# Kernel tuning notes

Hardware: AMD Instinct MI355X
Metric: run time of the kernel (lower is better)

The kernel has to match this reference:

```python
import jax, jax.numpy as jnp
import numpy as np

N = 50000      # nodes
E = 600000     # edges
HID = 128      # hidden_dim
H = 8          # attn_heads
D = HID // H   # attn_dim = 16
CLAMP = 5.0
LN_EPS = 1e-5


def _xavier(key, shape, fan_in, fan_out):
    std = float(np.sqrt(2.0 / (fan_in + fan_out)))
    return jax.random.normal(key, shape, dtype=jnp.float32) * std


def setup_inputs() -> dict:
    key = jax.random.key(0)
    ks = jax.random.split(key, 32)
    x = jax.random.normal(ks[0], (N, HID), dtype=jnp.float32)
    conn = jax.random.normal(ks[1], (E, HID), dtype=jnp.float32)
    log_deg = jax.random.uniform(ks[2], (N, 1), dtype=jnp.float32) * 4.0
    edge_index = jax.random.randint(ks[3], (2, E), 0, N)
    # attention projections (torch Linear weight [out,in]; stored here as [in,out])
    WQ = _xavier(ks[4], (HID, HID), HID, HID)
    WK = _xavier(ks[5], (HID, HID), HID, HID)
    WV = _xavier(ks[6], (HID, HID), HID, HID)
    WE = _xavier(ks[7], (HID, 2 * HID), HID, 2 * HID)
    Aw = _xavier(ks[8], (D, H, 1), D, 1)
    Bw = _xavier(ks[9], (D, H, D), D, D)
    Ho_w = _xavier(ks[10], (HID, HID), HID, HID)
    Ho_b = jnp.zeros((HID,), jnp.float32)
    Eo_w = _xavier(ks[11], (HID, HID), HID, HID)
    Eo_b = jnp.zeros((HID,), jnp.float32)
    deg_coef = _xavier(ks[12], (1, HID, 2), HID, 2)
    ln1h_g = jnp.ones((HID,), jnp.float32); ln1h_b = jnp.zeros((HID,), jnp.float32)
    ln1e_g = jnp.ones((HID,), jnp.float32); ln1e_b = jnp.zeros((HID,), jnp.float32)
    ln2h_g = jnp.ones((HID,), jnp.float32); ln2h_b = jnp.zeros((HID,), jnp.float32)
    W1 = _xavier(ks[13], (HID, 2 * HID), HID, 2 * HID)
    b1 = jnp.zeros((2 * HID,), jnp.float32)
    W2 = _xavier(ks[14], (2 * HID, HID), 2 * HID, HID)
    b2 = jnp.zeros((HID,), jnp.float32)
    return dict(x=x, conn=conn, log_deg=log_deg, edge_index=edge_index,
                WQ=WQ, WK=WK, WV=WV, WE=WE, Aw=Aw, Bw=Bw,
                Ho_w=Ho_w, Ho_b=Ho_b, Eo_w=Eo_w, Eo_b=Eo_b, deg_coef=deg_coef,
                ln1h_g=ln1h_g, ln1h_b=ln1h_b, ln1e_g=ln1e_g, ln1e_b=ln1e_b,
                ln2h_g=ln2h_g, ln2h_b=ln2h_b, W1=W1, b1=b1, W2=W2, b2=b2)


def _signed_sqrt(c):
    # sqrt(relu(c)) - sqrt(relu(-c)), written nan-safe for grads
    pos = jnp.sqrt(jnp.where(c > 0, c, 1.0))
    neg = jnp.sqrt(jnp.where(c < 0, -c, 1.0))
    return jnp.where(c > 0, pos, 0.0) - jnp.where(c < 0, neg, 0.0)


def _layernorm(v, g, b):
    m = jnp.mean(v, axis=-1, keepdims=True)
    var = jnp.mean(jnp.square(v - m), axis=-1, keepdims=True)
    return (v - m) * jax.lax.rsqrt(var + LN_EPS) * g + b


def _forward(x, conn, log_deg, edge_index, WQ, WK, WV, WE, Aw, Bw,
             Ho_w, Ho_b, Eo_w, Eo_b, deg_coef,
             ln1h_g, ln1h_b, ln1e_g, ln1e_b, ln2h_g, ln2h_b, W1, b1, W2, b2):
    dst, src = edge_index[0], edge_index[1]
    Qh = x @ WQ          # [N, HID]
    Kh = x @ WK
    Vh = x @ WV
    Eh = conn @ WE       # [E, 2*HID]
    Ew, Eb = Eh[:, :HID], Eh[:, HID:]

    msg1 = Qh[dst] + Kh[src]                 # gather  [E, HID]
    conn_e = jax.nn.relu(_signed_sqrt(msg1 * Ew) + Eb)   # act='relu'
    e_attn = conn_e                          # Eo (edge output of attention)

    conn_r = conn_e.reshape(E, H, D)
    score = jnp.einsum('ehd,dhc->ehc', conn_r, Aw)       # [E, H, 1]
    score = jnp.clip(score, -CLAMP, CLAMP)
    # scatter softmax over dst
    smax = jax.ops.segment_max(score, dst, num_segments=N)
    score = jnp.exp(score - smax[dst])
    ssum = jax.ops.segment_sum(score, dst, num_segments=N)
    score = score / (ssum[dst] + 1e-16)

    Vsrc = Vh[src].reshape(E, H, D)
    agg = jax.ops.segment_sum(Vsrc * score, dst, num_segments=N)   # [N, H, D]
    rowV = jax.ops.segment_sum(conn_r * score, dst, num_segments=N)
    rowV = jnp.einsum('nhd,dhc->nhc', rowV, Bw)                    # [N, H, D]
    h_attn = Qh + (agg + rowV).reshape(N, HID)

    # outer layer (eval mode: no dropout)
    h = jnp.stack([h_attn, h_attn * log_deg], axis=-1)   # [N, HID, 2]
    h = jnp.sum(h * deg_coef, axis=-1)
    h = h @ Ho_w + Ho_b
    e = e_attn @ Eo_w + Eo_b
    h = x + h
    e = conn + e
    h = _layernorm(h, ln1h_g, ln1h_b)
    e = _layernorm(e, ln1e_g, ln1e_b)
    h_in2 = h
    h = jax.nn.relu(h @ W1 + b1) @ W2 + b2
    h = _layernorm(h_in2 + h, ln2h_g, ln2h_b)
    return h, e


def reference(x, conn, log_deg, edge_index, WQ, WK, WV, WE, Aw, Bw,
              Ho_w, Ho_b, Eo_w, Eo_b, deg_coef,
              ln1h_g, ln1h_b, ln1e_g, ln1e_b, ln2h_g, ln2h_b, W1, b1, W2, b2):
    return _forward(x, conn, log_deg, edge_index, WQ, WK, WV, WE, Aw, Bw,
                    Ho_w, Ho_b, Eo_w, Eo_b, deg_coef,
                    ln1h_g, ln1h_b, ln1e_g, ln1e_b, ln2h_g, ln2h_b, W1, b1, W2, b2)
```

## Files before the change

### kernel.cpp

```cpp
#include <hip/hip_runtime.h>
#include <hip/hip_bf16.h>

#define NN 50000
#define NE 600000
#define HIDC 128
#define NH 8
#define DH 16

typedef unsigned short u16;
typedef __attribute__((ext_vector_type(8))) short bf16x8;
typedef __attribute__((ext_vector_type(4))) float f32x4;

static __device__ __forceinline__ float bf2f(u16 u) {
    unsigned int x = ((unsigned int)u) << 16;
    return __uint_as_float(x);
}
static __device__ __forceinline__ u16 f2bf(float f) {
    unsigned int x = __float_as_uint(f);
    unsigned int r = (x + 0x7fffu + ((x >> 16) & 1u)) >> 16;
    return (u16)r;
}
static __device__ __forceinline__ void split2(float v, u16& h, u16& l) {
    h = f2bf(v);
    l = f2bf(v - bf2f(h));
}

__global__ void k_init(int* deg, int* cursor) {
    int i = blockIdx.x * blockDim.x + threadIdx.x;
    if (i < NN) { deg[i] = 0; cursor[i] = 0; }
}

__global__ void k_count(const int* __restrict__ ei, int* __restrict__ deg) {
    int e = blockIdx.x * blockDim.x + threadIdx.x;
    if (e < NE) atomicAdd(&deg[ei[e]], 1);
}

__global__ void k_scan(const int* __restrict__ deg, int* __restrict__ rowstart) {
    __shared__ int warpsum[16];
    __shared__ int chunkcarry;
    int t = threadIdx.x;
    int lane = t & 63, w = t >> 6;
    if (t == 0) { chunkcarry = 0; rowstart[0] = 0; }
    __syncthreads();
    for (int base = 0; base < NN; base += 4096) {
        int idx = base + t * 4;
        int v0 = (idx + 0 < NN) ? deg[idx + 0] : 0;
        int v1 = (idx + 1 < NN) ? deg[idx + 1] : 0;
        int v2 = (idx + 2 < NN) ? deg[idx + 2] : 0;
        int v3 = (idx + 3 < NN) ? deg[idx + 3] : 0;
        int s0 = v0, s1 = s0 + v1, s2 = s1 + v2, s3 = s2 + v3;
        int tot = s3;
        int sc = tot;
#pragma unroll
        for (int off = 1; off < 64; off <<= 1) {
            int u = __shfl_up(sc, off);
            if (lane >= off) sc += u;
        }
        if (lane == 63) warpsum[w] = sc;
        __syncthreads();
        int wpre = 0;
        for (int i = 0; i < w; i++) wpre += warpsum[i];
        int carry = chunkcarry;
        __syncthreads();
        int pre = carry + wpre + (sc - tot);
        if (idx + 0 < NN) rowstart[idx + 1] = pre + s0;
        if (idx + 1 < NN) rowstart[idx + 2] = pre + s1;
        if (idx + 2 < NN) rowstart[idx + 3] = pre + s2;
        if (idx + 3 < NN) rowstart[idx + 4] = pre + s3;
        if (t == 1023) chunkcarry = carry + wpre + sc;
        __syncthreads();
    }
}

__global__ void k_fill(const int* __restrict__ ei, const int* __restrict__ rowstart,
                       int* __restrict__ cursor, int* __restrict__ csr) {
    int e = blockIdx.x * blockDim.x + threadIdx.x;
    if (e < NE) {
        int d = ei[e];
        int slot = atomicAdd(&cursor[d], 1);
        csr[rowstart[d] + slot] = e;
    }
}

template <int NC, int K, bool RELU>
__global__ __launch_bounds__(256) void k_gemm(const float* __restrict__ A,
                                              const float* __restrict__ W,
                                              const float* __restrict__ bias,
                                              float* __restrict__ C, int M) {
    constexpr int NCT_W = NC / 32;
    __shared__ __align__(16) u16 Ah[4 * 64 * 8], Al[4 * 64 * 8];
    __shared__ __align__(16) u16 Bh[(NC / 16) * 64 * 8], Bl[(NC / 16) * 64 * 8];

    const int t = threadIdx.x;
    const int lane = t & 63, wid = t >> 6;
    const int wr = wid >> 1, wc = wid & 1;
    const int c15 = lane & 15, lg = lane >> 4;
    const int row0 = blockIdx.x * 64;

    f32x4 acc[2][NCT_W];
#pragma unroll
    for (int m = 0; m < 2; m++)
#pragma unroll
        for (int n = 0; n < NCT_W; n++) acc[m][n] = (f32x4){0.f, 0.f, 0.f, 0.f};

    for (int k0 = 0; k0 < K; k0 += 32) {
#pragma unroll
        for (int i = 0; i < 2; i++) {
            int fl = t * 2 + i;
            int r = fl >> 3, k4 = fl & 7;
            float4 v = make_float4(0.f, 0.f, 0.f, 0.f);
            int row = row0 + r;
            if (row < M) v = *(const float4*)(A + (size_t)row * K + k0 + k4 * 4);
            int base = ((r >> 4) * 64 + (r & 15) + ((k4 >> 1) << 4)) * 8 + (k4 & 1) * 4;
            u16 hx, lx, hy, ly, hz, lz, hw, lw;
            split2(v.x, hx, lx); split2(v.y, hy, ly);
            split2(v.z, hz, lz); split2(v.w, hw, lw);
            ushort4 ph; ph.x = hx; ph.y = hy; ph.z = hz; ph.w = hw;
            ushort4 pl; pl.x = lx; pl.y = ly; pl.z = lz; pl.w = lw;
            *(ushort4*)&Ah[base] = ph;
            *(ushort4*)&Al[base] = pl;
        }
#pragma unroll
        for (int hb = 0; hb < NC / 128; hb++) {
            int kb = (t >> 5) * 4;
            int c0 = hb * 128 + (t & 31) * 4;
            const float* wp = W + (size_t)(k0 + kb) * NC + c0;
            float4 w0 = *(const float4*)(wp);
            float4 w1 = *(const float4*)(wp + NC);
            float4 w2 = *(const float4*)(wp + 2 * NC);
            float4 w3 = *(const float4*)(wp + 3 * NC);
#pragma unroll
            for (int j = 0; j < 4; j++) {
                float e0 = j == 0 ? w0.x : j == 1 ? w0.y : j == 2 ? w0.z : w0.w;
                float e1 = j == 0 ? w1.x : j == 1 ? w1.y : j == 2 ? w1.z : w1.w;
                float e2 = j == 0 ? w2.x : j == 1 ? w2.y : j == 2 ? w2.z : w2.w;
                float e3 = j == 0 ? w3.x : j == 1 ? w3.y : j == 2 ? w3.z : w3.w;
                int c = c0 + j;
                int base = ((c >> 4) * 64 + (c & 15) + ((kb >> 3) << 4)) * 8 + (kb & 4);
                u16 h0, l0, h1, l1, h2, l2, h3, l3;
                split2(e0, h0, l0); split2(e1, h1, l1);
                split2(e2, h2, l2); split2(e3, h3, l3);
                ushort4 ph; ph.x = h0; ph.y = h1; ph.z = h2; ph.w = h3;
                ushort4 pl; pl.x = l0; pl.y = l1; pl.z = l2; pl.w = l3;
                *(ushort4*)&Bh[base] = ph;
                *(ushort4*)&Bl[base] = pl;
            }
        }
        __syncthreads();
        bf16x8 ah[2], alo[2];
#pragma unroll
        for (int m = 0; m < 2; m++) {
            int rt = wr * 2 + m;
            ah[m] = *(const bf16x8*)&Ah[(rt * 64 + lane) * 8];
            alo[m] = *(const bf16x8*)&Al[(rt * 64 + lane) * 8];
        }
#pragma unroll
        for (int n = 0; n < NCT_W; n++) {
            int ct = wc * NCT_W + n;
            bf16x8 bh = *(const bf16x8*)&Bh[(ct * 64 + lane) * 8];
            bf16x8 bl = *(const bf16x8*)&Bl[(ct * 64 + lane) * 8];
#pragma unroll
            for (int m = 0; m < 2; m++) {
                acc[m][n] = __builtin_amdgcn_mfma_f32_16x16x32_bf16(ah[m], bh, acc[m][n], 0, 0, 0);
                acc[m][n] = __builtin_amdgcn_mfma_f32_16x16x32_bf16(ah[m], bl, acc[m][n], 0, 0, 0);
                acc[m][n] = __builtin_amdgcn_mfma_f32_16x16x32_bf16(alo[m], bh, acc[m][n], 0, 0, 0);
            }
        }
        __syncthreads();
    }
#pragma unroll
    for (int m = 0; m < 2; m++) {
        int rbase = row0 + wr * 32 + m * 16 + lg * 4;
#pragma unroll
        for (int n = 0; n < NCT_W; n++) {
            int col = wc * (NCT_W * 16) + n * 16 + c15;
            float bv = bias ? bias[col] : 0.f;
#pragma unroll
            for (int r = 0; r < 4; r++) {
                int row = rbase + r;
                if (row < M) {
                    float o = acc[m][n][r] + bv;
                    if (RELU) o = fmaxf(o, 0.f);
                    C[(size_t)row * NC + col] = o;
                }
            }
        }
    }
}

__global__ __launch_bounds__(256) void k_edge_pre(
    const float* __restrict__ conn, const float* __restrict__ WE,
    const float* __restrict__ Qh, const float* __restrict__ Kh,
    const int* __restrict__ ei, const float* __restrict__ Aw,
    u16* __restrict__ conn_e, float* __restrict__ scoreraw) {
    __shared__ __align__(16) u16 Ah[4 * 64 * 8], Al[4 * 64 * 8];
    __shared__ __align__(16) u16 Bh[16 * 64 * 8], Bl[16 * 64 * 8];
    const int t = threadIdx.x;
    const int lane = t & 63, wid = t >> 6;
    const int wr = wid >> 1, wc = wid & 1;
    const int c15 = lane & 15, lg = lane >> 4;
    const int row0 = blockIdx.x * 64;

    f32x4 acc[2][8];
#pragma unroll
    for (int m = 0; m < 2; m++)
#pragma unroll
        for (int n = 0; n < 8; n++) acc[m][n] = (f32x4){0.f, 0.f, 0.f, 0.f};

    for (int k0 = 0; k0 < 128; k0 += 32) {
#pragma unroll
        for (int i = 0; i < 2; i++) {
            int fl = t * 2 + i;
            int r = fl >> 3, k4 = fl & 7;
            float4 v = *(const float4*)(conn + (size_t)(row0 + r) * 128 + k0 + k4 * 4);
            int base = ((r >> 4) * 64 + (r & 15) + ((k4 >> 1) << 4)) * 8 + (k4 & 1) * 4;
            u16 hx, lx, hy, ly, hz, lz, hw, lw;
            split2(v.x, hx, lx); split2(v.y, hy, ly);
            split2(v.z, hz, lz); split2(v.w, hw, lw);
            ushort4 ph; ph.x = hx; ph.y = hy; ph.z = hz; ph.w = hw;
            ushort4 pl; pl.x = lx; pl.y = ly; pl.z = lz; pl.w = lw;
            *(ushort4*)&Ah[base] = ph;
            *(ushort4*)&Al[base] = pl;
        }
#pragma unroll
        for (int hb = 0; hb < 2; hb++) {
            int kb = (t >> 5) * 4;
            int c0 = hb * 128 + (t & 31) * 4;
            const float* wp = WE + (size_t)(k0 + kb) * 256 + c0;
            float4 w0 = *(const float4*)(wp);
            float4 w1 = *(const float4*)(wp + 256);
            float4 w2 = *(const float4*)(wp + 512);
            float4 w3 = *(const float4*)(wp + 768);
#pragma unroll
            for (int j = 0; j < 4; j++) {
                float e0 = j == 0 ? w0.x : j == 1 ? w0.y : j == 2 ? w0.z : w0.w;
                float e1 = j == 0 ? w1.x : j == 1 ? w1.y : j == 2 ? w1.z : w1.w;
                float e2 = j == 0 ? w2.x : j == 1 ? w2.y : j == 2 ? w2.z : w2.w;
                float e3 = j == 0 ? w3.x : j == 1 ? w3.y : j == 2 ? w3.z : w3.w;
                int c = c0 + j;
                int base = ((c >> 4) * 64 + (c & 15) + ((kb >> 3) << 4)) * 8 + (kb & 4);
                u16 h0, l0, h1, l1, h2, l2, h3, l3;
                split2(e0, h0, l0); split2(e1, h1, l1);
                split2(e2, h2, l2); split2(e3, h3, l3);
                ushort4 ph; ph.x = h0; ph.y = h1; ph.z = h2; ph.w = h3;
                ushort4 pl; pl.x = l0; pl.y = l1; pl.z = l2; pl.w = l3;
                *(ushort4*)&Bh[base] = ph;
                *(ushort4*)&Bl[base] = pl;
            }
        }
        __syncthreads();
        bf16x8 ah[2], alo[2];
#pragma unroll
        for (int m = 0; m < 2; m++) {
            int rt = wr * 2 + m;
            ah[m] = *(const bf16x8*)&Ah[(rt * 64 + lane) * 8];
            alo[m] = *(const bf16x8*)&Al[(rt * 64 + lane) * 8];
        }
#pragma unroll
        for (int nn = 0; nn < 8; nn++) {
            int ct = (nn < 4) ? (wc * 4 + nn) : (8 + wc * 4 + (nn - 4));
            bf16x8 bh = *(const bf16x8*)&Bh[(ct * 64 + lane) * 8];
            bf16x8 bl = *(const bf16x8*)&Bl[(ct * 64 + lane) * 8];
#pragma unroll
            for (int m = 0; m < 2; m++) {
                acc[m][nn] = __builtin_amdgcn_mfma_f32_16x16x32_bf16(ah[m], bh, acc[m][nn], 0, 0, 0);
                acc[m][nn] = __builtin_amdgcn_mfma_f32_16x16x32_bf16(ah[m], bl, acc[m][nn], 0, 0, 0);
                acc[m][nn] = __builtin_amdgcn_mfma_f32_16x16x32_bf16(alo[m], bh, acc[m][nn], 0, 0, 0);
            }
        }
        __syncthreads();
    }

    float aw0 = Aw[c15 * 8 + wc * 4 + 0];
    float aw1 = Aw[c15 * 8 + wc * 4 + 1];
    float aw2 = Aw[c15 * 8 + wc * 4 + 2];
    float aw3 = Aw[c15 * 8 + wc * 4 + 3];

#pragma unroll
    for (int m = 0; m < 2; m++) {
#pragma unroll
        for (int r = 0; r < 4; r++) {
            int e = row0 + wr * 32 + m * 16 + lg * 4 + r;
            int dn = ei[e], sn = ei[NE + e];
            float sp0 = 0.f, sp1 = 0.f, sp2 = 0.f, sp3 = 0.f;
#pragma unroll
            for (int n = 0; n < 4; n++) {
                int j = wc * 64 + n * 16 + c15;
                float mv = Qh[(size_t)dn * 128 + j] + Kh[(size_t)sn * 128 + j];
                float cw = mv * acc[m][n][r];
                float ss = (cw > 0.f) ? sqrtf(cw) : ((cw < 0.f) ? -sqrtf(-cw) : 0.f);
                float v = fmaxf(ss + acc[m][4 + n][r], 0.f);
                conn_e[(size_t)e * 128 + j] = f2bf(v);
                float aw = n == 0 ? aw0 : n == 1 ? aw1 : n == 2 ? aw2 : aw3;
                float s = v * aw;
                s += __shfl_xor(s, 1);
                s += __shfl_xor(s, 2);
                s += __shfl_xor(s, 4);
                s += __shfl_xor(s, 8);
                if (n == 0) sp0 = s; else if (n == 1) sp1 = s; else if (n == 2) sp2 = s; else sp3 = s;
            }
            if (c15 == 0) {
                size_t sb = (size_t)e * 8 + wc * 4;
                scoreraw[sb + 0] = fminf(fmaxf(sp0, -5.f), 5.f);
                scoreraw[sb + 1] = fminf(fmaxf(sp1, -5.f), 5.f);
                scoreraw[sb + 2] = fminf(fmaxf(sp2, -5.f), 5.f);
                scoreraw[sb + 3] = fminf(fmaxf(sp3, -5.f), 5.f);
            }
        }
    }
}

__global__ void k_gather(const int* __restrict__ ei, const int* __restrict__ rowstart,
                         const int* __restrict__ csr, const float* __restrict__ scoreraw,
                         const u16* __restrict__ conn_e, const float* __restrict__ Vh,
                         const float* __restrict__ Qh, const float* __restrict__ Bw,
                         const float* __restrict__ logdeg, const float* __restrict__ deg_coef,
                         float* __restrict__ tout) {
    int n = blockIdx.x;
    int j = threadIdx.x;
    int h = j >> 4, d = j & 15;
    int rs = rowstart[n], re = rowstart[n + 1];

    float mx = -1e30f;
    for (int p = rs; p < re; p++) {
        int e = csr[p];
        mx = fmaxf(mx, scoreraw[(size_t)e * 8 + h]);
    }
    float ssum = 0.f, aggj = 0.f, rowvj = 0.f;
    for (int p = rs; p < re; p++) {
        int e = csr[p];
        float s = expf(scoreraw[(size_t)e * 8 + h] - mx);
        ssum += s;
        int sn = ei[NE + e];
        aggj = fmaf(Vh[(size_t)sn * 128 + j], s, aggj);
        rowvj = fmaf(bf2f(conn_e[(size_t)e * 128 + j]), s, rowvj);
    }
    float inv = 1.f / (ssum + 1e-16f);
    aggj *= inv;
    rowvj *= inv;

    __shared__ float rv[128];
    rv[j] = rowvj;
    __syncthreads();
    float ro = 0.f;
#pragma unroll
    for (int d2 = 0; d2 < 16; d2++) ro = fmaf(rv[h * 16 + d2], Bw[(d2 * 8 + h) * 16 + d], ro);

    float ha = Qh[(size_t)n * 128 + j] + aggj + ro;
    float ld = logdeg[n];
    tout[(size_t)n * 128 + j] = ha * (deg_coef[2 * j] + ld * deg_coef[2 * j + 1]);
}

__global__ void k_ln_res(const float* __restrict__ a, const float* __restrict__ b,
                         const float* __restrict__ g, const float* __restrict__ be,
                         float* __restrict__ out, int M) {
    int row = blockIdx.x * 4 + (threadIdx.x >> 6);
    int lane = threadIdx.x & 63;
    if (row >= M) return;
    size_t off = (size_t)row * 128 + lane * 2;
    float v0 = a[off] + b[off];
    float v1 = a[off + 1] + b[off + 1];
    float s = v0 + v1;
#pragma unroll
    for (int m = 1; m < 64; m <<= 1) s += __shfl_xor(s, m);
    float mean = s * (1.f / 128.f);
    float d0 = v0 - mean, d1 = v1 - mean;
    float q = d0 * d0 + d1 * d1;
#pragma unroll
    for (int m = 1; m < 64; m <<= 1) q += __shfl_xor(q, m);
    float rstd = rsqrtf(q * (1.f / 128.f) + 1e-5f);
    out[off] = d0 * rstd * g[lane * 2] + be[lane * 2];
    out[off + 1] = d1 * rstd * g[lane * 2 + 1] + be[lane * 2 + 1];
}

__global__ __launch_bounds__(256) void k_edge_out(
    const u16* __restrict__ conn_e, const float* __restrict__ Eo_w,
    const float* __restrict__ Eo_b, const float* __restrict__ conn,
    const float* __restrict__ g, const float* __restrict__ be,
    float* __restrict__ eout) {
    __shared__ __align__(16) u16 Asm[4 * 64 * 8];
    __shared__ __align__(16) u16 Bh[8 * 64 * 8], Bl[8 * 64 * 8];
    const int t = threadIdx.x;
    const int lane = t & 63, wid = t >> 6;
    const int c15 = lane & 15, lg = lane >> 4;
    const int row0 = blockIdx.x * 64;

    f32x4 acc[8];
#pragma unroll
    for (int n = 0; n < 8; n++) acc[n] = (f32x4){0.f, 0.f, 0.f, 0.f};

    for (int k0 = 0; k0 < 128; k0 += 32) {
        {
            int r = t >> 2, gq = t & 3;
            uint4 u = *(const uint4*)(conn_e + (size_t)(row0 + r) * 128 + k0 + gq * 8);
            int base = ((r >> 4) * 64 + (r & 15) + (gq << 4)) * 8;
            *(uint4*)&Asm[base] = u;
        }
        {
            int kb = (t >> 5) * 4;
            int c0 = (t & 31) * 4;
            const float* wp = Eo_w + (size_t)(k0 + kb) * 128 + c0;
            float4 w0 = *(const float4*)(wp);
            float4 w1 = *(const float4*)(wp + 128);
            float4 w2 = *(const float4*)(wp + 256);
            float4 w3 = *(const float4*)(wp + 384);
#pragma unroll
            for (int j = 0; j < 4; j++) {
                float e0 = j == 0 ? w0.x : j == 1 ? w0.y : j == 2 ? w0.z : w0.w;
                float e1 = j == 0 ? w1.x : j == 1 ? w1.y : j == 2 ? w1.z : w1.w;
                float e2 = j == 0 ? w2.x : j == 1 ? w2.y : j == 2 ? w2.z : w2.w;
                float e3 = j == 0 ? w3.x : j == 1 ? w3.y : j == 2 ? w3.z : w3.w;
                int c = c0 + j;
                int base = ((c >> 4) * 64 + (c & 15) + ((kb >> 3) << 4)) * 8 + (kb & 4);
                u16 h0, l0, h1, l1, h2, l2, h3, l3;
                split2(e0, h0, l0); split2(e1, h1, l1);
                split2(e2, h2, l2); split2(e3, h3, l3);
                ushort4 ph; ph.x = h0; ph.y = h1; ph.z = h2; ph.w = h3;
                ushort4 pl; pl.x = l0; pl.y = l1; pl.z = l2; pl.w = l3;
                *(ushort4*)&Bh[base] = ph;
                *(ushort4*)&Bl[base] = pl;
            }
        }
        __syncthreads();
        bf16x8 a = *(const bf16x8*)&Asm[(wid * 64 + lane) * 8];
#pragma unroll
        for (int n = 0; n < 8; n++) {
            bf16x8 bh = *(const bf16x8*)&Bh[(n * 64 + lane) * 8];
            bf16x8 bl = *(const bf16x8*)&Bl[(n * 64 + lane) * 8];
            acc[n] = __builtin_amdgcn_mfma_f32_16x16x32_bf16(a, bh, acc[n], 0, 0, 0);
            acc[n] = __builtin_amdgcn_mfma_f32_16x16x32_bf16(a, bl, acc[n], 0, 0, 0);
        }
        __syncthreads();
    }

    float ebv[8], gv[8], bev[8];
#pragma unroll
    for (int n = 0; n < 8; n++) {
        int col = n * 16 + c15;
        ebv[n] = Eo_b[col];
        gv[n] = g[col];
        bev[n] = be[col];
    }
#pragma unroll
    for (int r = 0; r < 4; r++) {
        int e = row0 + wid * 16 + lg * 4 + r;
        float v[8];
        float s1 = 0.f, s2 = 0.f;
#pragma unroll
        for (int n = 0; n < 8; n++) {
            int col = n * 16 + c15;
            float x = acc[n][r] + ebv[n] + conn[(size_t)e * 128 + col];
            v[n] = x;
            s1 += x;
            s2 += x * x;
        }
#pragma unroll
        for (int msk = 1; msk < 16; msk <<= 1) {
            s1 += __shfl_xor(s1, msk);
            s2 += __shfl_xor(s2, msk);
        }
        float mean = s1 * (1.f / 128.f);
        float var = s2 * (1.f / 128.f) - mean * mean;
        float rstd = rsqrtf(var + 1e-5f);
#pragma unroll
        for (int n = 0; n < 8; n++) {
            int col = n * 16 + c15;
            eout[(size_t)e * 128 + col] = (v[n] - mean) * rstd * gv[n] + bev[n];
        }
    }
}

extern "C" void kernel_launch(void* const* d_in, const int* in_sizes, int n_in,
                              void* d_out, int out_size, void* d_ws, size_t ws_size,
                              hipStream_t stream) {
    const float* x = (const float*)d_in[0];
    const float* conn = (const float*)d_in[1];
    const float* log_deg = (const float*)d_in[2];
    const int* ei = (const int*)d_in[3];
    const float* WQ = (const float*)d_in[4];
    const float* WK = (const float*)d_in[5];
    const float* WV = (const float*)d_in[6];
    const float* WE = (const float*)d_in[7];
    const float* Aw = (const float*)d_in[8];
    const float* Bw = (const float*)d_in[9];
    const float* Ho_w = (const float*)d_in[10];
    const float* Ho_b = (const float*)d_in[11];
    const float* Eo_w = (const float*)d_in[12];
    const float* Eo_b = (const float*)d_in[13];
    const float* deg_coef = (const float*)d_in[14];
    const float* ln1h_g = (const float*)d_in[15];
    const float* ln1h_b = (const float*)d_in[16];
    const float* ln1e_g = (const float*)d_in[17];
    const float* ln1e_b = (const float*)d_in[18];
    const float* ln2h_g = (const float*)d_in[19];
    const float* ln2h_b = (const float*)d_in[20];
    const float* W1 = (const float*)d_in[21];
    const float* b1 = (const float*)d_in[22];
    const float* W2 = (const float*)d_in[23];
    const float* b2 = (const float*)d_in[24];

    float* fbase = (float*)d_ws;
    float* Qh = fbase;
    float* Kh = Qh + (size_t)NN * HIDC;
    float* Vh = Kh + (size_t)NN * HIDC;
    float* tbuf = Vh + (size_t)NN * HIDC;
    float* h1 = tbuf + (size_t)NN * HIDC;
    float* scoreraw = h1 + (size_t)NN * HIDC;
    u16* conn_e = (u16*)(scoreraw + (size_t)NE * NH);
    int* deg = (int*)(conn_e + (size_t)NE * HIDC);
    int* rowstart = deg + NN;
    int* cursor = rowstart + NN + 1;
    int* csr = cursor + NN;
    float* f1 = (float*)conn_e;
    float* u_h = Vh;
    float* u2 = Qh;

    float* out_h = (float*)d_out;
    float* out_e = out_h + (size_t)NN * HIDC;

    const int gN64 = (NN + 63) / 64;
    const int gE64 = NE / 64;

    k_init<<<(NN + 255) / 256, 256, 0, stream>>>(deg, cursor);
    k_count<<<(NE + 255) / 256, 256, 0, stream>>>(ei, deg);
    k_scan<<<1, 1024, 0, stream>>>(deg, rowstart);
    k_fill<<<(NE + 255) / 256, 256, 0, stream>>>(ei, rowstart, cursor, csr);

    k_gemm<128, 128, false><<<gN64, 256, 0, stream>>>(x, WQ, nullptr, Qh, NN);
    k_gemm<128, 128, false><<<gN64, 256, 0, stream>>>(x, WK, nullptr, Kh, NN);
    k_gemm<128, 128, false><<<gN64, 256, 0, stream>>>(x, WV, nullptr, Vh, NN);

    k_edge_pre<<<gE64, 256, 0, stream>>>(conn, WE, Qh, Kh, ei, Aw, conn_e, scoreraw);

    k_gather<<<NN, 128, 0, stream>>>(ei, rowstart, csr, scoreraw, conn_e, Vh, Qh, Bw,
                                     log_deg, deg_coef, tbuf);

    k_gemm<128, 128, false><<<gN64, 256, 0, stream>>>(tbuf, Ho_w, Ho_b, u_h, NN);
    k_ln_res<<<(NN + 3) / 4, 256, 0, stream>>>(u_h, x, ln1h_g, ln1h_b, h1, NN);

    k_edge_out<<<gE64, 256, 0, stream>>>(conn_e, Eo_w, Eo_b, conn, ln1e_g, ln1e_b, out_e);

    k_gemm<256, 128, true><<<gN64, 256, 0, stream>>>(h1, W1, b1, f1, NN);
    k_gemm<128, 256, false><<<gN64, 256, 0, stream>>>(f1, W2, b2, u2, NN);
    k_ln_res<<<(NN + 3) / 4, 256, 0, stream>>>(u2, h1, ln2h_g, ln2h_b, out_h, NN);
}
```

Measured before the change: 1.642 ms.

## Pre-split weights into bf16 hi/lo MFMA layout once and pack two nodes per gather block

Adds a small kernel that converts each weight matrix once into pre-swizzled bf16 hi/lo tiles. The GEMM, edge_pre and edge_out kernels then copy those tiles straight into shared memory with uint4 loads, so every block no longer re-splits the weights. The A-tile staging now writes 8 values per thread as 16-byte stores. The gather kernel handles two nodes per 256-thread block instead of one node per 128-thread block. The cost is eight extra tiny launches and extra workspace, which must not overlap the existing buffers.

```diff
diff --git a/kernel.cpp b/kernel.cpp
--- a/kernel.cpp
+++ b/kernel.cpp
@@ -82,14 +82,37 @@
     }
 }
 
+__global__ void k_conv_w(const float* __restrict__ W, u16* __restrict__ hi,
+                         u16* __restrict__ lo, int K, int NC) {
+    int idx = blockIdx.x * blockDim.x + threadIdx.x;
+    int total = (K >> 5) * (NC >> 4) * 64;
+    if (idx >= total) return;
+    int l = idx & 63;
+    int f = idx >> 6;
+    int NCT = NC >> 4;
+    int kt = f / NCT, ct = f - kt * NCT;
+    int col = ct * 16 + (l & 15);
+    int krow = kt * 32 + (l >> 4) * 8;
+    u16 ph[8], pl[8];
+#pragma unroll
+    for (int j = 0; j < 8; j++) {
+        float v = W[(size_t)(krow + j) * NC + col];
+        split2(v, ph[j], pl[j]);
+    }
+    *(uint4*)(hi + (size_t)idx * 8) = *(uint4*)ph;
+    *(uint4*)(lo + (size_t)idx * 8) = *(uint4*)pl;
+}
+
 template <int NC, int K, bool RELU>
 __global__ __launch_bounds__(256) void k_gemm(const float* __restrict__ A,
-                                              const float* __restrict__ W,
+                                              const u16* __restrict__ Wh,
+                                              const u16* __restrict__ Wl,
                                               const float* __restrict__ bias,
                                               float* __restrict__ C, int M) {
+    constexpr int NCT = NC / 16;
     constexpr int NCT_W = NC / 32;
     __shared__ __align__(16) u16 Ah[4 * 64 * 8], Al[4 * 64 * 8];
-    __shared__ __align__(16) u16 Bh[(NC / 16) * 64 * 8], Bl[(NC / 16) * 64 * 8];
+    __shared__ __align__(16) u16 Bh[NCT * 64 * 8], Bl[NCT * 64 * 8];
 
     const int t = threadIdx.x;
     const int lane = t & 63, wid = t >> 6;
@@ -103,47 +126,33 @@
 #pragma unroll
         for (int n = 0; n < NCT_W; n++) acc[m][n] = (f32x4){0.f, 0.f, 0.f, 0.f};
 
-    for (int k0 = 0; k0 < K; k0 += 32) {
-#pragma unroll
-        for (int i = 0; i < 2; i++) {
-            int fl = t * 2 + i;
-            int r = fl >> 3, k4 = fl & 7;
-            float4 v = make_float4(0.f, 0.f, 0.f, 0.f);
+    for (int kt = 0; kt < K / 32; kt++) {
+        {
+            int r = t >> 2, ko = t & 3;
             int row = row0 + r;
-            if (row < M) v = *(const float4*)(A + (size_t)row * K + k0 + k4 * 4);
-            int base = ((r >> 4) * 64 + (r & 15) + ((k4 >> 1) << 4)) * 8 + (k4 & 1) * 4;
-            u16 hx, lx, hy, ly, hz, lz, hw, lw;
-            split2(v.x, hx, lx); split2(v.y, hy, ly);
-            split2(v.z, hz, lz); split2(v.w, hw, lw);
-            ushort4 ph; ph.x = hx; ph.y = hy; ph.z = hz; ph.w = hw;
-            ushort4 pl; pl.x = lx; pl.y = ly; pl.z = lz; pl.w = lw;
-            *(ushort4*)&Ah[base] = ph;
-            *(ushort4*)&Al[base] = pl;
-        }
-#pragma unroll
-        for (int hb = 0; hb < NC / 128; hb++) {
-            int kb = (t >> 5) * 4;
-            int c0 = hb * 128 + (t & 31) * 4;
-            const float* wp = W + (size_t)(k0 + kb) * NC + c0;
-            float4 w0 = *(const float4*)(wp);
-            float4 w1 = *(const float4*)(wp + NC);
-            float4 w2 = *(const float4*)(wp + 2 * NC);
-            float4 w3 = *(const float4*)(wp + 3 * NC);
-#pragma unroll
-            for (int j = 0; j < 4; j++) {
-                float e0 = j == 0 ? w0.x : j == 1 ? w0.y : j == 2 ? w0.z : w0.w;
-                float e1 = j == 0 ? w1.x : j == 1 ? w1.y : j == 2 ? w1.z : w1.w;
-                float e2 = j == 0 ? w2.x : j == 1 ? w2.y : j == 2 ? w2.z : w2.w;
-                float e3 = j == 0 ? w3.x : j == 1 ? w3.y : j == 2 ? w3.z : w3.w;
-                int c = c0 + j;
-                int base = ((c >> 4) * 64 + (c & 15) + ((kb >> 3) << 4)) * 8 + (kb & 4);
-                u16 h0, l0, h1, l1, h2, l2, h3, l3;
-                split2(e0, h0, l0); split2(e1, h1, l1);
-                split2(e2, h2, l2); split2(e3, h3, l3);
-                ushort4 ph; ph.x = h0; ph.y = h1; ph.z = h2; ph.w = h3;
-                ushort4 pl; pl.x = l0; pl.y = l1; pl.z = l2; pl.w = l3;
-                *(ushort4*)&Bh[base] = ph;
-                *(ushort4*)&Bl[base] = pl;
+            float4 v0 = make_float4(0.f, 0.f, 0.f, 0.f), v1 = v0;
+            if (row < M) {
+                const float* ap = A + (size_t)row * K + kt * 32 + ko * 8;
+                v0 = *(const float4*)ap;
+                v1 = *(const float4*)(ap + 4);
+            }
+            u16 ph[8], pl[8];
+            split2(v0.x, ph[0], pl[0]); split2(v0.y, ph[1], pl[1]);
+            split2(v0.z, ph[2], pl[2]); split2(v0.w, ph[3], pl[3]);
+            split2(v1.x, ph[4], pl[4]); split2(v1.y, ph[5], pl[5]);
+            split2(v1.z, ph[6], pl[6]); split2(v1.w, ph[7], pl[7]);
+            int ab = ((r >> 4) * 64 + ko * 16 + (r & 15)) * 8;
+            *(uint4*)&Ah[ab] = *(uint4*)ph;
+            *(uint4*)&Al[ab] = *(uint4*)pl;
+        }
+        {
+            const u16* bhp = Wh + (size_t)kt * (NCT * 512);
+            const u16* blp = Wl + (size_t)kt * (NCT * 512);
+#pragma unroll
+            for (int i = 0; i < NCT / 4; i++) {
+                int o = (t + i * 256) * 8;
+                *(uint4*)&Bh[o] = *(const uint4*)&bhp[o];
+                *(uint4*)&Bl[o] = *(const uint4*)&blp[o];
             }
         }
         __syncthreads();
@@ -189,7 +198,7 @@
 }
 
 __global__ __launch_bounds__(256) void k_edge_pre(
-    const float* __restrict__ conn, const float* __restrict__ WE,
+    const float* __restrict__ conn, const u16* __restrict__ WEh, const u16* __restrict__ WEl,
     const float* __restrict__ Qh, const float* __restrict__ Kh,
     const int* __restrict__ ei, const float* __restrict__ Aw,
     u16* __restrict__ conn_e, float* __restrict__ scoreraw) {
@@ -207,45 +216,29 @@
 #pragma unroll
         for (int n = 0; n < 8; n++) acc[m][n] = (f32x4){0.f, 0.f, 0.f, 0.f};
 
-    for (int k0 = 0; k0 < 128; k0 += 32) {
-#pragma unroll
-        for (int i = 0; i < 2; i++) {
-            int fl = t * 2 + i;
-            int r = fl >> 3, k4 = fl & 7;
-            float4 v = *(const float4*)(conn + (size_t)(row0 + r) * 128 + k0 + k4 * 4);
-            int base = ((r >> 4) * 64 + (r & 15) + ((k4 >> 1) << 4)) * 8 + (k4 & 1) * 4;
-            u16 hx, lx, hy, ly, hz, lz, hw, lw;
-            split2(v.x, hx, lx); split2(v.y, hy, ly);
-            split2(v.z, hz, lz); split2(v.w, hw, lw);
-            ushort4 ph; ph.x = hx; ph.y = hy; ph.z = hz; ph.w = hw;
-            ushort4 pl; pl.x = lx; pl.y = ly; pl.z = lz; pl.w = lw;
-            *(ushort4*)&Ah[base] = ph;
-            *(ushort4*)&Al[base] = pl;
-        }
-#pragma unroll
-        for (int hb = 0; hb < 2; hb++) {
-            int kb = (t >> 5) * 4;
-            int c0 = hb * 128 + (t & 31) * 4;
-            const float* wp = WE + (size_t)(k0 + kb) * 256 + c0;
-            float4 w0 = *(const float4*)(wp);
-            float4 w1 = *(const float4*)(wp + 256);
-            float4 w2 = *(const float4*)(wp + 512);
-            float4 w3 = *(const float4*)(wp + 768);
-#pragma unroll
-            for (int j = 0; j < 4; j++) {
-                float e0 = j == 0 ? w0.x : j == 1 ? w0.y : j == 2 ? w0.z : w0.w;
-                float e1 = j == 0 ? w1.x : j == 1 ? w1.y : j == 2 ? w1.z : w1.w;
-                float e2 = j == 0 ? w2.x : j == 1 ? w2.y : j == 2 ? w2.z : w2.w;
-                float e3 = j == 0 ? w3.x : j == 1 ? w3.y : j == 2 ? w3.z : w3.w;
-                int c = c0 + j;
-                int base = ((c >> 4) * 64 + (c & 15) + ((kb >> 3) << 4)) * 8 + (kb & 4);
-                u16 h0, l0, h1, l1, h2, l2, h3, l3;
-                split2(e0, h0, l0); split2(e1, h1, l1);
-                split2(e2, h2, l2); split2(e3, h3, l3);
-                ushort4 ph; ph.x = h0; ph.y = h1; ph.z = h2; ph.w = h3;
-                ushort4 pl; pl.x = l0; pl.y = l1; pl.z = l2; pl.w = l3;
-                *(ushort4*)&Bh[base] = ph;
-                *(ushort4*)&Bl[base] = pl;
+    for (int kt = 0; kt < 4; kt++) {
+        {
+            int r = t >> 2, ko = t & 3;
+            const float* ap = conn + (size_t)(row0 + r) * 128 + kt * 32 + ko * 8;
+            float4 v0 = *(const float4*)ap;
+            float4 v1 = *(const float4*)(ap + 4);
+            u16 ph[8], pl[8];
+            split2(v0.x, ph[0], pl[0]); split2(v0.y, ph[1], pl[1]);
+            split2(v0.z, ph[2], pl[2]); split2(v0.w, ph[3], pl[3]);
+            split2(v1.x, ph[4], pl[4]); split2(v1.y, ph[5], pl[5]);
+            split2(v1.z, ph[6], pl[6]); split2(v1.w, ph[7], pl[7]);
+            int ab = ((r >> 4) * 64 + ko * 16 + (r & 15)) * 8;
+            *(uint4*)&Ah[ab] = *(uint4*)ph;
+            *(uint4*)&Al[ab] = *(uint4*)pl;
+        }
+        {
+            const u16* bhp = WEh + (size_t)kt * (16 * 512);
+            const u16* blp = WEl + (size_t)kt * (16 * 512);
+#pragma unroll
+            for (int i = 0; i < 4; i++) {
+                int o = (t + i * 256) * 8;
+                *(uint4*)&Bh[o] = *(const uint4*)&bhp[o];
+                *(uint4*)&Bl[o] = *(const uint4*)&blp[o];
             }
         }
         __syncthreads();
@@ -316,8 +309,9 @@
                          const float* __restrict__ Qh, const float* __restrict__ Bw,
                          const float* __restrict__ logdeg, const float* __restrict__ deg_coef,
                          float* __restrict__ tout) {
-    int n = blockIdx.x;
-    int j = threadIdx.x;
+    int half = threadIdx.x >> 7;
+    int n = blockIdx.x * 2 + half;
+    int j = threadIdx.x & 127;
     int h = j >> 4, d = j & 15;
     int rs = rowstart[n], re = rowstart[n + 1];
 
@@ -339,12 +333,12 @@
     aggj *= inv;
     rowvj *= inv;
 
-    __shared__ float rv[128];
-    rv[j] = rowvj;
+    __shared__ float rv[2][128];
+    rv[half][j] = rowvj;
     __syncthreads();
     float ro = 0.f;
 #pragma unroll
-    for (int d2 = 0; d2 < 16; d2++) ro = fmaf(rv[h * 16 + d2], Bw[(d2 * 8 + h) * 16 + d], ro);
+    for (int d2 = 0; d2 < 16; d2++) ro = fmaf(rv[half][h * 16 + d2], Bw[(d2 * 8 + h) * 16 + d], ro);
 
     float ha = Qh[(size_t)n * 128 + j] + aggj + ro;
     float ld = logdeg[n];
@@ -374,7 +368,7 @@
 }
 
 __global__ __launch_bounds__(256) void k_edge_out(
-    const u16* __restrict__ conn_e, const float* __restrict__ Eo_w,
+    const u16* __restrict__ conn_e, const u16* __restrict__ Eoh, const u16* __restrict__ Eol,
     const float* __restrict__ Eo_b, const float* __restrict__ conn,
     const float* __restrict__ g, const float* __restrict__ be,
     float* __restrict__ eout) {
@@ -389,36 +383,21 @@
 #pragma unroll
     for (int n = 0; n < 8; n++) acc[n] = (f32x4){0.f, 0.f, 0.f, 0.f};
 
-    for (int k0 = 0; k0 < 128; k0 += 32) {
+    for (int kt = 0; kt < 4; kt++) {
         {
             int r = t >> 2, gq = t & 3;
-            uint4 u = *(const uint4*)(conn_e + (size_t)(row0 + r) * 128 + k0 + gq * 8);
+            uint4 u = *(const uint4*)(conn_e + (size_t)(row0 + r) * 128 + kt * 32 + gq * 8);
             int base = ((r >> 4) * 64 + (r & 15) + (gq << 4)) * 8;
             *(uint4*)&Asm[base] = u;
         }
         {
-            int kb = (t >> 5) * 4;
-            int c0 = (t & 31) * 4;
-            const float* wp = Eo_w + (size_t)(k0 + kb) * 128 + c0;
-            float4 w0 = *(const float4*)(wp);
-            float4 w1 = *(const float4*)(wp + 128);
-            float4 w2 = *(const float4*)(wp + 256);
-            float4 w3 = *(const float4*)(wp + 384);
-#pragma unroll
-            for (int j = 0; j < 4; j++) {
-                float e0 = j == 0 ? w0.x : j == 1 ? w0.y : j == 2 ? w0.z : w0.w;
-                float e1 = j == 0 ? w1.x : j == 1 ? w1.y : j == 2 ? w1.z : w1.w;
-                float e2 = j == 0 ? w2.x : j == 1 ? w2.y : j == 2 ? w2.z : w2.w;
-                float e3 = j == 0 ? w3.x : j == 1 ? w3.y : j == 2 ? w3.z : w3.w;
-                int c = c0 + j;
-                int base = ((c >> 4) * 64 + (c & 15) + ((kb >> 3) << 4)) * 8 + (kb & 4);
-                u16 h0, l0, h1, l1, h2, l2, h3, l3;
-                split2(e0, h0, l0); split2(e1, h1, l1);
-                split2(e2, h2, l2); split2(e3, h3, l3);
-                ushort4 ph; ph.x = h0; ph.y = h1; ph.z = h2; ph.w = h3;
-                ushort4 pl; pl.x = l0; pl.y = l1; pl.z = l2; pl.w = l3;
-                *(ushort4*)&Bh[base] = ph;
-                *(ushort4*)&Bl[base] = pl;
+            const u16* bhp = Eoh + (size_t)kt * (8 * 512);
+            const u16* blp = Eol + (size_t)kt * (8 * 512);
+#pragma unroll
+            for (int i = 0; i < 2; i++) {
+                int o = (t + i * 256) * 8;
+                *(uint4*)&Bh[o] = *(const uint4*)&bhp[o];
+                *(uint4*)&Bl[o] = *(const uint4*)&blp[o];
             }
         }
         __syncthreads();
@@ -515,32 +494,51 @@
     float* u_h = Vh;
     float* u2 = Qh;
 
+    u16* wbuf = (u16*)(((uintptr_t)(csr + NE) + 15) & ~(uintptr_t)15);
+    u16* WQh = wbuf;            u16* WQl = WQh + 16384;
+    u16* WKh = WQl + 16384;     u16* WKl = WKh + 16384;
+    u16* WVh = WKl + 16384;     u16* WVl = WVh + 16384;
+    u16* WEh = WVl + 16384;     u16* WEl = WEh + 32768;
+    u16* Hoh = WEl + 32768;     u16* Hol = Hoh + 16384;
+    u16* Eoh = Hol + 16384;     u16* Eol = Eoh + 16384;
+    u16* W1h = Eol + 16384;     u16* W1l = W1h + 32768;
+    u16* W2h = W1l + 32768;     u16* W2l = W2h + 32768;
+
     float* out_h = (float*)d_out;
     float* out_e = out_h + (size_t)NN * HIDC;
 
     const int gN64 = (NN + 63) / 64;
     const int gE64 = NE / 64;
+
+    k_conv_w<<<(2048 + 255) / 256, 256, 0, stream>>>(WQ, WQh, WQl, 128, 128);
+    k_conv_w<<<(2048 + 255) / 256, 256, 0, stream>>>(WK, WKh, WKl, 128, 128);
+    k_conv_w<<<(2048 + 255) / 256, 256, 0, stream>>>(WV, WVh, WVl, 128, 128);
+    k_conv_w<<<(4096 + 255) / 256, 256, 0, stream>>>(WE, WEh, WEl, 128, 256);
+    k_conv_w<<<(2048 + 255) / 256, 256, 0, stream>>>(Ho_w, Hoh, Hol, 128, 128);
+    k_conv_w<<<(2048 + 255) / 256, 256, 0, stream>>>(Eo_w, Eoh, Eol, 128, 128);
+    k_conv_w<<<(4096 + 255) / 256, 256, 0, stream>>>(W1, W1h, W1l, 128, 256);
+    k_conv_w<<<(4096 + 255) / 256, 256, 0, stream>>>(W2, W2h, W2l, 256, 128);
 
     k_init<<<(NN + 255) / 256, 256, 0, stream>>>(deg, cursor);
     k_count<<<(NE + 255) / 256, 256, 0, stream>>>(ei, deg);
     k_scan<<<1, 1024, 0, stream>>>(deg, rowstart);
     k_fill<<<(NE + 255) / 256, 256, 0, stream>>>(ei, rowstart, cursor, csr);
 
-    k_gemm<128, 128, false><<<gN64, 256, 0, stream>>>(x, WQ, nullptr, Qh, NN);
-    k_gemm<128, 128, false><<<gN64, 256, 0, stream>>>(x, WK, nullptr, Kh, NN);
-    k_gemm<128, 128, false><<<gN64, 256, 0, stream>>>(x, WV, nullptr, Vh, NN);
-
-    k_edge_pre<<<gE64, 256, 0, stream>>>(conn, WE, Qh, Kh, ei, Aw, conn_e, scoreraw);
-
-    k_gather<<<NN, 128, 0, stream>>>(ei, rowstart, csr, scoreraw, conn_e, Vh, Qh, Bw,
-                                     log_deg, deg_coef, tbuf);
-
-    k_gemm<128, 128, false><<<gN64, 256, 0, stream>>>(tbuf, Ho_w, Ho_b, u_h, NN);
+    k_gemm<128, 128, false><<<gN64, 256, 0, stream>>>(x, WQh, WQl, nullptr, Qh, NN);
+    k_gemm<128, 128, false><<<gN64, 256, 0, stream>>>(x, WKh, WKl, nullptr, Kh, NN);
+    k_gemm<128, 128, false><<<gN64, 256, 0, stream>>>(x, WVh, WVl, nullptr, Vh, NN);
+
+    k_edge_pre<<<gE64, 256, 0, stream>>>(conn, WEh, WEl, Qh, Kh, ei, Aw, conn_e, scoreraw);
+
+    k_gather<<<NN / 2, 256, 0, stream>>>(ei, rowstart, csr, scoreraw, conn_e, Vh, Qh, Bw,
+                                         log_deg, deg_coef, tbuf);
+
+    k_gemm<128, 128, false><<<gN64, 256, 0, stream>>>(tbuf, Hoh, Hol, Ho_b, u_h, NN);
     k_ln_res<<<(NN + 3) / 4, 256, 0, stream>>>(u_h, x, ln1h_g, ln1h_b, h1, NN);
 
-    k_edge_out<<<gE64, 256, 0, stream>>>(conn_e, Eo_w, Eo_b, conn, ln1e_g, ln1e_b, out_e);
-
-    k_gemm<256, 128, true><<<gN64, 256, 0, stream>>>(h1, W1, b1, f1, NN);
-    k_gemm<128, 256, false><<<gN64, 256, 0, stream>>>(f1, W2, b2, u2, NN);
+    k_edge_out<<<gE64, 256, 0, stream>>>(conn_e, Eoh, Eol, Eo_b, conn, ln1e_g, ln1e_b, out_e);
+
+    k_gemm<256, 128, true><<<gN64, 256, 0, stream>>>(h1, W1h, W1l, b1, f1, NN);
+    k_gemm<128, 256, false><<<gN64, 256, 0, stream>>>(f1, W2h, W2l, b2, u2, NN);
     k_ln_res<<<(NN + 3) / 4, 256, 0, stream>>>(u2, h1, ln2h_g, ln2h_b, out_h, NN);
 }
```

Measured after the change: 1.569 ms. 1.05x faster.
